# Kernel optimization log

Measured on AMD Instinct MI355X. Metric: run time of the kernel, lower is better.

## Reference

```python
import jax, jax.numpy as jnp
import numpy as np

B = 1024
IN_H, IN_W = 128, 128
KH, KW = 10, 10
SH, SW = 5, 5
PH, PW = 2, 2
HP, WP = IN_H + 2 * PH, IN_W + 2 * PW          # padded dims: 132, 132
NKH = (IN_H - KH + 2 * PH) // SH + 1            # 25
NKW = (IN_W - KW + 2 * PW) // SW + 1            # 25
NK = NKH * NKW                                  # 625


def _build_weight_matrix(kernel_weights):
    """kernel_weights: [NK, KH, KW] -> sparse-structured dense [HP*WP, NK].
    Faithful to LocallyConnected2dV2._create_weight_matrix, vectorized."""
    i = jnp.arange(NK)
    start_i = (i // NKW) * SH                   # [NK]
    start_j = (i % NKW) * SW                    # [NK]
    # flat row index for each (kernel, k, l) tap in padded image
    rows = ((start_i[:, None, None] + jnp.arange(KH)[None, :, None]) * WP
            + start_j[:, None, None] + jnp.arange(KW)[None, None, :])  # [NK,KH,KW]
    rows = rows.reshape(NK, KH * KW)
    cols = i[:, None]                           # [NK,1] broadcasts over taps
    W = jnp.zeros((HP * WP, NK), dtype=kernel_weights.dtype)
    return W.at[rows, cols].set(kernel_weights.reshape(NK, KH * KW))


def setup_inputs() -> dict:
    key = jax.random.key(0)
    kx, kw, kb = jax.random.split(key, 3)
    x = jax.random.normal(kx, (B, IN_H, IN_W), dtype=jnp.float32)
    kernel_weights = jax.random.normal(kw, (NK, KH, KW), dtype=jnp.float32)
    W = _build_weight_matrix(kernel_weights)    # [HP*WP, NK]
    bias = jax.random.normal(kb, (NKH, NKW), dtype=jnp.float32)
    return {"x": x, "W": W, "bias": bias}


def reference(x, W, bias):
    # zero-pad spatial dims, flatten, dense GEMM against sparse-structured W
    xp = jnp.pad(x, ((0, 0), (PH, PH), (PW, PW)))          # [B,HP,WP]
    xf = xp.reshape(x.shape[0], HP * WP)                   # [B,HP*WP]
    out = xf @ W                                           # [B,NK]
    out = out.reshape(x.shape[0], NKH, NKW)
    return out + bias
```

## Files before the change

### kernel.cpp

```cpp
#include <hip/hip_runtime.h>

typedef _Float16 f16x2 __attribute__((ext_vector_type(2)));
typedef __fp16  fp16x2 __attribute__((ext_vector_type(2)));

constexpr int NKW  = 25, NK = 625;
constexpr int WPADR = 132;
constexpr int WPT   = 160;
constexpr int RST   = 35;
constexpr int BROWS = 30;
constexpr int BITEM = BROWS * 32;
constexpr int NBAND = 5;

union U2H { unsigned int u; f16x2 h; fp16x2 p; };

__global__ void gather_wp(const float* __restrict__ W, _Float16* __restrict__ wgpT) {
    int t = blockIdx.x * 256 + threadIdx.x;
    if (t >= NK * WPT) return;
    int k = t / WPT, p = t % WPT;
    int di = p >> 4, s = p & 15;
    int ki = k / NKW, kj = k % NKW;
    int o = (5 * kj + 2) & 3;
    int j = s - o;
    float val = 0.f;
    if (j >= 0 && j < 10)
        val = W[(size_t)((ki * 5 + di) * WPADR + kj * 5 + j) * NK + k];
    wgpT[((size_t)(p >> 3) * NK + k) * 8 + (p & 7)] = (_Float16)val;
}

__device__ __forceinline__ float dot2acc(unsigned int a, unsigned int b, float c) {
    U2H ua, ub; ua.u = a; ub.u = b;
#if __has_builtin(__builtin_amdgcn_fdot2)
    return __builtin_amdgcn_fdot2(ua.h, ub.h, c, false);
#else
    return c + (float)ua.h.x * (float)ub.h.x + (float)ua.h.y * (float)ub.h.y;
#endif
}

template <bool USE_WG>
__global__ __launch_bounds__(256, 4)
void lc2d_band(const float* __restrict__ x, const _Float16* __restrict__ wgpT,
               const float* __restrict__ Wfull,
               const float* __restrict__ bias, float* __restrict__ out) {
    __shared__ uint2 xs[2][BROWS * RST];

    const int b    = blockIdx.x;
    const int tid  = threadIdx.x;
    const int lane = tid & 63;
    const int pairidx = (tid >> 6) * 32 + (lane & 31);
    const int half = lane >> 5;
    const int di0  = half * 5;
    const bool active = pairidx < 125;
    const int ki_l = pairidx / 25;
    const int kj   = pairidx - ki_l * 25;
    const float* xb = x + ((size_t)b << 14);

    float4 tmp[4];
    auto band_load = [&](int t) {
        const int r0 = 25 * t - 2;
#pragma unroll
        for (int u = 0; u < 4; ++u) {
            const int i = tid + u * 256;
            tmp[u] = make_float4(0.f, 0.f, 0.f, 0.f);
            if (i < BITEM) {
                const int r = r0 + (i >> 5), q = i & 31;
                if (r >= 0 && r < 128)
                    tmp[u] = *reinterpret_cast<const float4*>(xb + (r << 7) + (q << 2));
            }
        }
    };
    auto band_write = [&](int buf) {
#pragma unroll
        for (int u = 0; u < 4; ++u) {
            const int i = tid + u * 256;
            if (i < BITEM) {
                const int idx = i >> 5, q = (i & 31) + 1;
                U2H u0h, u1h;
                u0h.p = __builtin_amdgcn_cvt_pkrtz(tmp[u].x, tmp[u].y);
                u1h.p = __builtin_amdgcn_cvt_pkrtz(tmp[u].z, tmp[u].w);
                xs[buf][idx * RST + q] = make_uint2(u0h.u, u1h.u);
            }
        }
    };

    uint4 wq[10];
    float bv = 0.f;
    auto load_w = [&](int t) {
        if (!active) return;
        const int k = 125 * t + pairidx;
        if constexpr (USE_WG) {
            const uint4* wt4 = reinterpret_cast<const uint4*>(wgpT);
#pragma unroll
            for (int j = 0; j < 10; ++j) wq[j] = wt4[(size_t)(half * 10 + j) * NK + k];
        } else {
            const int ki = 5 * t + ki_l;
            const int o = (5 * kj + 2) & 3;
#pragma unroll
            for (int j = 0; j < 10; ++j) {
                const int di = di0 + (j >> 1), pb = (j & 1) * 8;
                unsigned int uu[4];
#pragma unroll
                for (int m = 0; m < 4; ++m) {
                    float f0 = 0.f, f1 = 0.f;
                    const int j0 = pb + 2 * m - o, j1 = pb + 2 * m + 1 - o;
                    const size_t rowb = (size_t)((ki * 5 + di) * WPADR + kj * 5);
                    if (j0 >= 0 && j0 < 10) f0 = Wfull[(rowb + j0) * NK + k];
                    if (j1 >= 0 && j1 < 10) f1 = Wfull[(rowb + j1) * NK + k];
                    U2H u; u.p = __builtin_amdgcn_cvt_pkrtz(f0, f1);
                    uu[m] = u.u;
                }
                wq[j] = make_uint4(uu[0], uu[1], uu[2], uu[3]);
            }
        }
        if (half == 0) bv = bias[k];
    };

    auto compute = [&](int t, int buf) {
        float acc0 = 0.f, acc1 = 0.f;
        if (active) {
            const uint2* base = xs[buf] + (5 * ki_l + di0) * RST + ((5 * kj + 2) >> 2);
#pragma unroll
            for (int d = 0; d < 5; ++d) {
                const uint2* rowp = base + d * RST;
                const uint2 a0 = rowp[0], a1 = rowp[1], a2 = rowp[2], a3 = rowp[3];
                const uint4 wA = wq[2 * d], wB = wq[2 * d + 1];
                acc0 = dot2acc(a0.x, wA.x, acc0);
                acc1 = dot2acc(a0.y, wA.y, acc1);
                acc0 = dot2acc(a1.x, wA.z, acc0);
                acc1 = dot2acc(a1.y, wA.w, acc1);
                acc0 = dot2acc(a2.x, wB.x, acc0);
                acc1 = dot2acc(a2.y, wB.y, acc1);
                acc0 = dot2acc(a3.x, wB.z, acc0);
                acc1 = dot2acc(a3.y, wB.w, acc1);
            }
        }
        float acc = acc0 + acc1;
        float other = __shfl_xor(acc, 32, 64);
        if (active && half == 0)
            out[(size_t)b * NK + 125 * t + pairidx] = acc + other + bv;
    };

    for (int i = tid; i < 4 * BROWS; i += 256)
        xs[i & 1][(i >> 2) * RST + ((i >> 1) & 1) * 33] = make_uint2(0u, 0u);

    band_load(0);
    band_write(0);
    load_w(0);
    __syncthreads();

#pragma unroll
    for (int t = 0; t < NBAND; ++t) {
        if (t + 1 < NBAND) band_load(t + 1);
        compute(t, t & 1);
        if (t + 1 < NBAND) {
            load_w(t + 1);
            band_write((t + 1) & 1);
            __syncthreads();
        }
    }
}

extern "C" void kernel_launch(void* const* d_in, const int* in_sizes, int n_in,
                              void* d_out, int out_size, void* d_ws, size_t ws_size,
                              hipStream_t stream) {
    const float* x    = (const float*)d_in[0];
    const float* W    = (const float*)d_in[1];
    const float* bias = (const float*)d_in[2];
    float* out = (float*)d_out;

    const dim3 grid(1024);
    if (ws_size >= (size_t)NK * WPT * sizeof(_Float16)) {
        _Float16* wgpT = (_Float16*)d_ws;
        gather_wp<<<(NK * WPT + 255) / 256, 256, 0, stream>>>(W, wgpT);
        lc2d_band<true><<<grid, 256, 0, stream>>>(x, wgpT, W, bias, out);
    } else {
        lc2d_band<false><<<grid, 256, 0, stream>>>(x, nullptr, W, bias, out);
    }
}
```

Measured before the change: 127.7 us.

## Split each batch image across five blocks, one per row band

Instead of one block walking all five row bands of an image with a double-buffered LDS pipeline, each block now handles a single (image, band) pair, and the grid grows fivefold. This removes the in-block software pipeline and the double buffer, halving shared memory and dropping the launch-bounds occupancy hint, so more independent blocks can hide latency. In exchange, the overlapping halo rows between bands are loaded twice and each block pays its own setup cost.

```diff
diff --git a/kernel.cpp b/kernel.cpp
--- a/kernel.cpp
+++ b/kernel.cpp
@@ -37,13 +37,15 @@
 }
 
 template <bool USE_WG>
-__global__ __launch_bounds__(256, 4)
-void lc2d_band(const float* __restrict__ x, const _Float16* __restrict__ wgpT,
-               const float* __restrict__ Wfull,
-               const float* __restrict__ bias, float* __restrict__ out) {
-    __shared__ uint2 xs[2][BROWS * RST];
+__global__ __launch_bounds__(256)
+void lc2d_shard(const float* __restrict__ x, const _Float16* __restrict__ wgpT,
+                const float* __restrict__ Wfull,
+                const float* __restrict__ bias, float* __restrict__ out) {
+    __shared__ uint2 xs[BROWS * RST];
 
-    const int b    = blockIdx.x;
+    const int blk  = blockIdx.x;
+    const int b    = blk / NBAND;
+    const int t    = blk - b * NBAND;
     const int tid  = threadIdx.x;
     const int lane = tid & 63;
     const int pairidx = (tid >> 6) * 32 + (lane & 31);
@@ -55,7 +57,7 @@
     const float* xb = x + ((size_t)b << 14);
 
     float4 tmp[4];
-    auto band_load = [&](int t) {
+    {
         const int r0 = 25 * t - 2;
 #pragma unroll
         for (int u = 0; u < 4; ++u) {
@@ -67,25 +69,14 @@
                     tmp[u] = *reinterpret_cast<const float4*>(xb + (r << 7) + (q << 2));
             }
         }
-    };
-    auto band_write = [&](int buf) {
-#pragma unroll
-        for (int u = 0; u < 4; ++u) {
-            const int i = tid + u * 256;
-            if (i < BITEM) {
-                const int idx = i >> 5, q = (i & 31) + 1;
-                U2H u0h, u1h;
-                u0h.p = __builtin_amdgcn_cvt_pkrtz(tmp[u].x, tmp[u].y);
-                u1h.p = __builtin_amdgcn_cvt_pkrtz(tmp[u].z, tmp[u].w);
-                xs[buf][idx * RST + q] = make_uint2(u0h.u, u1h.u);
-            }
-        }
-    };
+    }
+
+    for (int i = tid; i < 2 * BROWS; i += 256)
+        xs[(i >> 1) * RST + (i & 1) * 33] = make_uint2(0u, 0u);
 
     uint4 wq[10];
     float bv = 0.f;
-    auto load_w = [&](int t) {
-        if (!active) return;
+    if (active) {
         const int k = 125 * t + pairidx;
         if constexpr (USE_WG) {
             const uint4* wt4 = reinterpret_cast<const uint4*>(wgpT);
@@ -112,51 +103,45 @@
             }
         }
         if (half == 0) bv = bias[k];
-    };
+    }
 
-    auto compute = [&](int t, int buf) {
-        float acc0 = 0.f, acc1 = 0.f;
-        if (active) {
-            const uint2* base = xs[buf] + (5 * ki_l + di0) * RST + ((5 * kj + 2) >> 2);
+    {
 #pragma unroll
-            for (int d = 0; d < 5; ++d) {
-                const uint2* rowp = base + d * RST;
-                const uint2 a0 = rowp[0], a1 = rowp[1], a2 = rowp[2], a3 = rowp[3];
-                const uint4 wA = wq[2 * d], wB = wq[2 * d + 1];
-                acc0 = dot2acc(a0.x, wA.x, acc0);
-                acc1 = dot2acc(a0.y, wA.y, acc1);
-                acc0 = dot2acc(a1.x, wA.z, acc0);
-                acc1 = dot2acc(a1.y, wA.w, acc1);
-                acc0 = dot2acc(a2.x, wB.x, acc0);
-                acc1 = dot2acc(a2.y, wB.y, acc1);
-                acc0 = dot2acc(a3.x, wB.z, acc0);
-                acc1 = dot2acc(a3.y, wB.w, acc1);
+        for (int u = 0; u < 4; ++u) {
+            const int i = tid + u * 256;
+            if (i < BITEM) {
+                const int idx = i >> 5, q = (i & 31) + 1;
+                U2H u0h, u1h;
+                u0h.p = __builtin_amdgcn_cvt_pkrtz(tmp[u].x, tmp[u].y);
+                u1h.p = __builtin_amdgcn_cvt_pkrtz(tmp[u].z, tmp[u].w);
+                xs[idx * RST + q] = make_uint2(u0h.u, u1h.u);
             }
         }
-        float acc = acc0 + acc1;
-        float other = __shfl_xor(acc, 32, 64);
-        if (active && half == 0)
-            out[(size_t)b * NK + 125 * t + pairidx] = acc + other + bv;
-    };
-
-    for (int i = tid; i < 4 * BROWS; i += 256)
-        xs[i & 1][(i >> 2) * RST + ((i >> 1) & 1) * 33] = make_uint2(0u, 0u);
-
-    band_load(0);
-    band_write(0);
-    load_w(0);
+    }
     __syncthreads();
 
+    float acc0 = 0.f, acc1 = 0.f;
+    if (active) {
+        const uint2* base = xs + (5 * ki_l + di0) * RST + ((5 * kj + 2) >> 2);
 #pragma unroll
-    for (int t = 0; t < NBAND; ++t) {
-        if (t + 1 < NBAND) band_load(t + 1);
-        compute(t, t & 1);
-        if (t + 1 < NBAND) {
-            load_w(t + 1);
-            band_write((t + 1) & 1);
-            __syncthreads();
+        for (int d = 0; d < 5; ++d) {
+            const uint2* rowp = base + d * RST;
+            const uint2 a0 = rowp[0], a1 = rowp[1], a2 = rowp[2], a3 = rowp[3];
+            const uint4 wA = wq[2 * d], wB = wq[2 * d + 1];
+            acc0 = dot2acc(a0.x, wA.x, acc0);
+            acc1 = dot2acc(a0.y, wA.y, acc1);
+            acc0 = dot2acc(a1.x, wA.z, acc0);
+            acc1 = dot2acc(a1.y, wA.w, acc1);
+            acc0 = dot2acc(a2.x, wB.x, acc0);
+            acc1 = dot2acc(a2.y, wB.y, acc1);
+            acc0 = dot2acc(a3.x, wB.z, acc0);
+            acc1 = dot2acc(a3.y, wB.w, acc1);
         }
     }
+    float acc = acc0 + acc1;
+    float other = __shfl_xor(acc, 32, 64);
+    if (active && half == 0)
+        out[(size_t)b * NK + 125 * t + pairidx] = acc + other + bv;
 }
 
 extern "C" void kernel_launch(void* const* d_in, const int* in_sizes, int n_in,
@@ -167,12 +152,12 @@
     const float* bias = (const float*)d_in[2];
     float* out = (float*)d_out;
 
-    const dim3 grid(1024);
+    const dim3 grid(1024 * NBAND);
     if (ws_size >= (size_t)NK * WPT * sizeof(_Float16)) {
         _Float16* wgpT = (_Float16*)d_ws;
         gather_wp<<<(NK * WPT + 255) / 256, 256, 0, stream>>>(W, wgpT);
-        lc2d_band<true><<<grid, 256, 0, stream>>>(x, wgpT, W, bias, out);
+        lc2d_shard<true><<<grid, 256, 0, stream>>>(x, wgpT, W, bias, out);
     } else {
-        lc2d_band<false><<<grid, 256, 0, stream>>>(x, nullptr, W, bias, out);
+        lc2d_shard<false><<<grid, 256, 0, stream>>>(x, nullptr, W, bias, out);
     }
 }
```

Measured after the change: 129.0 us. About the same (+1.0%).
